# Optimization experiments

Measured on AMD Instinct MI355X. Metric: run time of the kernel, lower is better.

## Reference

```python
import math
import jax, jax.numpy as jnp
import numpy as np

HEAD_DIM = 64
N_HEAD = 8
INIT_SIZE = 1200  # -> 1201 embeddings, origin_shift = 601


def rel_sinusoidal_pos_embed(seq_len, dim=HEAD_DIM):
    """Matches RelativeSinusoidalPositionalEmbedding(dim, padding_idx=0, init_size=1200)."""
    num = INIT_SIZE + 1  # 1201
    half = dim // 2
    inv_freq = jnp.exp(jnp.arange(half, dtype=jnp.float32) * -(math.log(10000.0) / (half - 1)))
    pos = jnp.arange(-(num // 2), num // 2, dtype=jnp.float32)  # -601 .. 599 (1201 values)
    ang = pos[:, None] * inv_freq[None, :]                      # [num, half]
    w = jnp.concatenate([jnp.sin(ang), jnp.cos(ang)], axis=1)   # [num, dim]
    w = w.at[0].set(0.0)  # padding_idx row zeroed
    origin_shift = num // 2 + 1  # 601
    idx = jnp.arange(-seq_len, seq_len) + origin_shift          # [2L]
    return w[idx]                                               # [2L, dim]


def _shift(BD):
    # BD: [b, n, L, 2L] -> [b, n, L, L] (Transformer-XL skew trick)
    b, n, L, _ = BD.shape
    BD = jnp.pad(BD, ((0, 0), (0, 0), (0, 0), (0, 1)))  # [b,n,L,2L+1]
    BD = BD.reshape(b, n, 2 * L + 1, L)[:, :, :-1].reshape(b, n, L, 2 * L)
    return BD[:, :, :, L:]


def _transpose_shift(E):
    # E: [b, n, L, 2L] -> [b, n, L, L]
    b, n, L, _ = E.shape
    E = jnp.pad(E, ((0, 0), (0, 0), (0, 0), (0, 1))).reshape(b, n, 2 * L + 1, L)
    idx = jnp.arange(L) * 2 + 1
    return jnp.swapaxes(E[:, :, idx, :], -1, -2)


def setup_inputs() -> dict:
    key = jax.random.key(0)
    k1, k2, k3, k4 = jax.random.split(key, 4)
    B, L, D = 8, 512, 512
    x = jax.random.normal(k1, (B, L, D), dtype=jnp.float32)
    mask = jnp.ones((B, L), dtype=jnp.int32)
    W_qkv = jax.random.normal(k2, (D, 3 * D), dtype=jnp.float32) * (1.0 / math.sqrt(D))
    r_r_bias = jax.random.normal(k3, (N_HEAD, HEAD_DIM), dtype=jnp.float32) * 0.1
    r_w_bias = jax.random.normal(k4, (N_HEAD, HEAD_DIM), dtype=jnp.float32) * 0.1
    return {"x": x, "mask": mask, "W_qkv": W_qkv, "r_r_bias": r_r_bias, "r_w_bias": r_w_bias}


def reference(x, mask, W_qkv, r_r_bias, r_w_bias):
    B, L, D = x.shape
    scale = math.sqrt(HEAD_DIM)
    pos = rel_sinusoidal_pos_embed(L)  # [2L, head_dim], detached constant

    qkv = x @ W_qkv  # [B, L, 3D]
    q, k, v = jnp.split(qkv, 3, axis=-1)
    q = q.reshape(B, L, N_HEAD, HEAD_DIM).transpose(0, 2, 1, 3)  # [B,H,L,d]
    k = k.reshape(B, L, N_HEAD, HEAD_DIM).transpose(0, 2, 1, 3)
    v = v.reshape(B, L, N_HEAD, HEAD_DIM).transpose(0, 2, 1, 3)

    rw_head_q = q + r_r_bias[None, :, None, :]
    AC = jnp.einsum('bnqd,bnkd->bnqk', rw_head_q, k)              # [B,H,L,L]
    D_ = jnp.einsum('nd,ld->nl', r_w_bias, pos)[None, :, None, :] # [1,H,1,2L]
    B_ = jnp.einsum('bnqd,ld->bnql', q, pos)                      # [B,H,L,2L]
    E_ = jnp.einsum('bnqd,ld->bnql', k, pos)                      # [B,H,L,2L]

    BDE = _shift(B_ + D_) + _transpose_shift(E_)                  # [B,H,L,L]
    attn = (AC + BDE) / scale
    attn = jnp.where(mask[:, None, None, :] == 0, -jnp.inf, attn)
    attn = jax.nn.softmax(attn, axis=-1)

    out = jnp.matmul(attn, v)                                     # [B,H,L,d]
    return out.transpose(0, 2, 1, 3).reshape(B, L, D)
```

## Files before the change

kernel.cpp:

```cpp
#include <hip/hip_runtime.h>
#include <hip/hip_bf16.h>
#include <math.h>

#define LSEQ 512
#define DDIM 192

typedef __attribute__((ext_vector_type(8))) short s16x8;
typedef __attribute__((ext_vector_type(4))) float f32x4;
typedef unsigned short ushort_t;
typedef unsigned int uint_t;

#define MFMA16(a, b, c) __builtin_amdgcn_mfma_f32_16x16x32_bf16(a, b, c, 0, 0, 0)

__device__ __forceinline__ ushort_t f2b(float f) {
  union { float f; uint_t u; } v; v.f = f;
  uint_t r = (v.u + 0x7FFFu + ((v.u >> 16) & 1u)) >> 16;
  return (ushort_t)r;
}
__device__ __forceinline__ float b2f(ushort_t u) {
  union { uint_t u; float f; } v; v.u = ((uint_t)u) << 16;
  return v.f;
}

typedef const __attribute__((address_space(1))) void g_void_t;
typedef __attribute__((address_space(3))) void lds_void_t;
__device__ __forceinline__ void load_lds16(const void* g, void* l) {
  __builtin_amdgcn_global_load_lds((g_void_t*)g, (lds_void_t*)l, 16, 0, 0);
}

__device__ __forceinline__ size_t kswz(size_t row, int d) {
  return row * DDIM + (size_t)((d & 0x1C7) | ((((d >> 3) & 7) ^ ((int)row & 7)) << 3));
}

__global__ void cast_x(const float* __restrict__ x, ushort_t* __restrict__ xb) {
  const int i = (blockIdx.x * 256 + threadIdx.x) * 8;
  const int row = i >> 9, k = i & 511;
  float4 a = *(const float4*)(x + i);
  float4 b = *(const float4*)(x + i + 4);
  uint4 o;
  o.x = (uint_t)f2b(a.x) | ((uint_t)f2b(a.y) << 16);
  o.y = (uint_t)f2b(a.z) | ((uint_t)f2b(a.w) << 16);
  o.z = (uint_t)f2b(b.x) | ((uint_t)f2b(b.y) << 16);
  o.w = (uint_t)f2b(b.z) | ((uint_t)f2b(b.w) << 16);
  const int dst = row * 512 + (k & 448) + (((((k >> 3) & 7) ^ (row & 7))) << 3);
  *(uint4*)(xb + dst) = o;
}

__global__ void cast_transpose_w(const float* __restrict__ W, ushort_t* __restrict__ Wt) {
  __shared__ float tile[32][33];
  const int tx = threadIdx.x & 31, ty = threadIdx.x >> 5;
  const int k0 = blockIdx.x * 32, n0 = blockIdx.y * 32;
#pragma unroll
  for (int i = 0; i < 4; ++i)
    tile[ty + i * 8][tx] = W[(size_t)(k0 + ty + i * 8) * 1536 + n0 + tx];
  __syncthreads();
#pragma unroll
  for (int i = 0; i < 4; ++i) {
    const int n = n0 + ty + i * 8, k = k0 + tx;
    Wt[(size_t)n * 512 + (k & 448) + ((((k >> 3) & 7) ^ (n & 7)) << 3) + (k & 7)] =
        f2b(tile[tx][ty + i * 8]);
  }
}

__global__ __launch_bounds__(256, 3) void qkv_gemm(
    const ushort_t* __restrict__ xb, const ushort_t* __restrict__ Wt,
    const float* __restrict__ rr,
    ushort_t* __restrict__ Qt, ushort_t* __restrict__ Kt, ushort_t* __restrict__ Vt) {
  __shared__ __align__(16) ushort_t ldsA[2][64 * 64];
  __shared__ __align__(16) ushort_t ldsB[2][128 * 64];
  const int tid = threadIdx.x;
  const int w = tid >> 6, lane = tid & 63, lo = lane & 15, hi = lane >> 4;
  const int wm = w >> 1, wn = w & 1;
  const int id = blockIdx.x;
  const int mp = id & 63, np = id >> 6;
  const int m0 = mp * 64, n0 = np * 128;

  f32x4 acc[2][4];
  const f32x4 zero4 = {0.f, 0.f, 0.f, 0.f};
#pragma unroll
  for (int i = 0; i < 2; ++i)
#pragma unroll
    for (int j = 0; j < 4; ++j) acc[i][j] = zero4;

  const char* asrc = (const char*)xb + (size_t)m0 * 1024;
  const char* bsrc = (const char*)Wt + (size_t)n0 * 1024;

#define STAGE_QKV(buf, ks)                                                     \
  {                                                                            \
    char* la = (char*)&ldsA[buf][0] + w * 1024;                                \
    char* lb = (char*)&ldsB[buf][0] + w * 1024;                                \
    _Pragma("unroll") for (int it = 0; it < 2; ++it) {                         \
      const int X = it * 4096 + tid * 16;                                      \
      load_lds16(asrc + (size_t)(X >> 7) * 1024 + (ks) * 128 + (X & 127),      \
                 la + it * 4096);                                              \
    }                                                                          \
    _Pragma("unroll") for (int it = 0; it < 4; ++it) {                         \
      const int X = it * 4096 + tid * 16;                                      \
      load_lds16(bsrc + (size_t)(X >> 7) * 1024 + (ks) * 128 + (X & 127),      \
                 lb + it * 4096);                                              \
    }                                                                          \
  }

  STAGE_QKV(0, 0);
  for (int ks = 0; ks < 8; ++ks) {
    const int cur = ks & 1;
    __syncthreads();
    if (ks < 7) STAGE_QKV(cur ^ 1, ks + 1);
    const char* Ab = (const char*)&ldsA[cur][0];
    const char* Bb = (const char*)&ldsB[cur][0];
#pragma unroll
    for (int kh = 0; kh < 2; ++kh) {
      const int sw = ((kh * 4 + hi) ^ (lo & 7)) << 4;
      s16x8 a[2], bf[4];
#pragma unroll
      for (int i = 0; i < 2; ++i)
        a[i] = *(const s16x8*)(Ab + (wm * 32 + i * 16 + lo) * 128 + sw);
#pragma unroll
      for (int j = 0; j < 4; ++j)
        bf[j] = *(const s16x8*)(Bb + (wn * 64 + j * 16 + lo) * 128 + sw);
#pragma unroll
      for (int i = 0; i < 2; ++i)
#pragma unroll
        for (int j = 0; j < 4; ++j)
          acc[i][j] = MFMA16(a[i], bf[j], acc[i][j]);
    }
  }

  const int sect = n0 >> 9;
  const int h = ((n0 + wn * 64) >> 6) & 7;
  const int mrow0 = m0 + wm * 32;

  if (sect == 0) {
    float bias[4];
#pragma unroll
    for (int j = 0; j < 4; ++j) bias[j] = rr[h * 64 + j * 16 + lo];
#pragma unroll
    for (int i = 0; i < 2; ++i)
#pragma unroll
      for (int r = 0; r < 4; ++r) {
        const int m = mrow0 + i * 16 + hi * 4 + r;
        const size_t row = ((size_t)(m >> 9) * 8 + h) * 512 + (m & 511);
#pragma unroll
        for (int j = 0; j < 4; ++j)
          Qt[row * DDIM + j * 16 + lo] = f2b((acc[i][j][r] + bias[j]) * 0.125f);
      }
  } else if (sect == 1) {
#pragma unroll
    for (int i = 0; i < 2; ++i)
#pragma unroll
      for (int r = 0; r < 4; ++r) {
        const int m = mrow0 + i * 16 + hi * 4 + r;
        const size_t row = ((size_t)(m >> 9) * 8 + h) * 512 + (m & 511);
#pragma unroll
        for (int j = 0; j < 4; ++j)
          Kt[row * DDIM + ((((j * 2 + (lo >> 3)) ^ (m & 7)) << 3) | (lo & 7))] =
              f2b(acc[i][j][r]);
      }
  } else {
#pragma unroll
    for (int i = 0; i < 2; ++i) {
      const int b = (mrow0 + i * 16) >> 9;
      const int l0 = (mrow0 + i * 16 + hi * 4) & 511;
#pragma unroll
      for (int j = 0; j < 4; ++j) {
        ushort4 pk;
        pk.x = f2b(acc[i][j][0]); pk.y = f2b(acc[i][j][1]);
        pk.z = f2b(acc[i][j][2]); pk.w = f2b(acc[i][j][3]);
        *(ushort4*)&Vt[(((size_t)b * 8 + h) * 64 + j * 16 + lo) * 512 + l0] = pk;
      }
    }
  }
}

__global__ void build_feats(ushort_t* __restrict__ Qt, ushort_t* __restrict__ Kt,
                            const float* __restrict__ rr, const float* __restrict__ rw) {
  const int idx = blockIdx.x * blockDim.x + threadIdx.x;
  const int hf = idx & 31;
  const size_t row = (size_t)(idx >> 5);
  const int l = (int)(row & 511);
  const int hh = (int)((row >> 9) & 7);

  const float f = __expf(-(float)hf * 0.29710775393472f);
  float s0, c0, s1, c1;
  __sincosf((float)l * f, &s0, &c0);
  __sincosf((float)(l + 1) * f, &s1, &c1);

  const size_t qb = row * DDIM;
  const float qr_s = b2f(Qt[qb + hf]);
  const float qr_c = b2f(Qt[qb + 32 + hf]);
  const float qw_s = qr_s + 0.125f * (rw[hh * 64 + hf] - rr[hh * 64 + hf]);
  const float qw_c = qr_c + 0.125f * (rw[hh * 64 + 32 + hf] - rr[hh * 64 + 32 + hf]);
  Qt[qb + 64 + hf]  = f2b(qw_s * c0 + qw_c * s0);
  Qt[qb + 96 + hf]  = f2b(qw_c * c0 - qw_s * s0);
  Qt[qb + 128 + hf] = f2b(0.125f * s1);
  Qt[qb + 160 + hf] = f2b(0.125f * c1);

  const float k_s = b2f(Kt[kswz(row, hf)]);
  const float k_c = b2f(Kt[kswz(row, 32 + hf)]);
  Kt[kswz(row, 64 + hf)]  = f2b(s1);
  Kt[kswz(row, 96 + hf)]  = f2b(c1);
  Kt[kswz(row, 128 + hf)] = f2b(k_s * c0 + k_c * s0);
  Kt[kswz(row, 160 + hf)] = f2b(k_c * c0 - k_s * s0);
}

__global__ __launch_bounds__(256, 2) void attn_kernel(
    const ushort_t* __restrict__ Qt, const ushort_t* __restrict__ Kt,
    const ushort_t* __restrict__ Vt, const int* __restrict__ mask,
    float* __restrict__ out) {
  __shared__ __align__(16) ushort_t ldsK[2][64 * DDIM];
  __shared__ __align__(16) ushort_t P[4][16][72];

  const int tid = threadIdx.x;
  const int w = tid >> 6;
  const int lane = tid & 63, lo = lane & 15, hi = lane >> 4;
  const int id = blockIdx.x;
  const int bh = id & 63, qg = id >> 6;
  const int b = bh >> 3, h = bh & 7;
  const int q0 = qg * 64 + w * 16;
  const size_t qrow0 = (size_t)bh * LSEQ + q0;

  s16x8 qf[6];
#pragma unroll
  for (int ks = 0; ks < 6; ++ks)
    qf[ks] = *(const s16x8*)(Qt + (qrow0 + lo) * DDIM + ks * 32 + hi * 8);

  const f32x4 zero4 = {0.f, 0.f, 0.f, 0.f};
  f32x4 o[4];
#pragma unroll
  for (int j = 0; j < 4; ++j) o[j] = zero4;
  float mrun = -3.0e38f, lrun = 0.f;

  const char* ksrc = (const char*)(Kt + (size_t)bh * LSEQ * DDIM);
  const ushort_t* vbase = Vt + ((size_t)bh * 64 + lo) * 512 + hi * 8;

  {
    char* d = (char*)&ldsK[0][0] + w * 1024;
#pragma unroll
    for (int it = 0; it < 6; ++it)
      load_lds16(ksrc + it * 4096 + tid * 16, d + it * 4096);
  }

  for (int kt = 0; kt < 8; ++kt) {
    const int cur = kt & 1;
    __syncthreads();
    if (kt < 7) {
      const char* s = ksrc + (kt + 1) * 24576;
      char* d = (char*)&ldsK[cur ^ 1][0] + w * 1024;
#pragma unroll
      for (int it = 0; it < 6; ++it)
        load_lds16(s + it * 4096 + tid * 16, d + it * 4096);
    }

    f32x4 sf[4];
#pragma unroll
    for (int f = 0; f < 4; ++f) sf[f] = zero4;
    const char* kl = (const char*)&ldsK[cur][0];
    __builtin_amdgcn_s_setprio(1);
#pragma unroll
    for (int ks = 0; ks < 6; ++ks) {
      const int swb = ((ks * 4 + hi) ^ (lo & 7)) << 4;
#pragma unroll
      for (int f = 0; f < 4; ++f) {
        s16x8 ka = *(const s16x8*)(kl + (f * 16 + lo) * 384 + swb);
        sf[f] = MFMA16(ka, qf[ks], sf[f]);
      }
    }
    __builtin_amdgcn_s_setprio(0);

    const int mk = mask[b * LSEQ + kt * 64 + lane];
    if (__ballot(mk == 0) != 0ull) {
#pragma unroll
      for (int f = 0; f < 4; ++f)
#pragma unroll
        for (int r = 0; r < 4; ++r)
          if (__shfl(mk, f * 16 + hi * 4 + r) == 0) sf[f][r] = -3.0e38f;
    }

    float tm = fmaxf(fmaxf(sf[0][0], sf[0][1]), fmaxf(sf[0][2], sf[0][3]));
#pragma unroll
    for (int f = 1; f < 4; ++f)
      tm = fmaxf(tm, fmaxf(fmaxf(sf[f][0], sf[f][1]), fmaxf(sf[f][2], sf[f][3])));
    tm = fmaxf(tm, __shfl_xor(tm, 16));
    tm = fmaxf(tm, __shfl_xor(tm, 32));

    if (!__all(tm - mrun <= 8.0f)) {
      const float mnew = fmaxf(mrun, tm);
      const float corr = __expf(mrun - mnew);
      lrun *= corr;
      mrun = mnew;
      float cq[4];
#pragma unroll
      for (int r = 0; r < 4; ++r) cq[r] = __shfl(corr, hi * 4 + r);
#pragma unroll
      for (int j = 0; j < 4; ++j)
#pragma unroll
        for (int r = 0; r < 4; ++r) o[j][r] *= cq[r];
    }

    float ts = 0.f;
#pragma unroll
    for (int f = 0; f < 4; ++f)
#pragma unroll
      for (int r = 0; r < 4; ++r) {
        sf[f][r] = __expf(sf[f][r] - mrun);
        ts += sf[f][r];
      }
    ts += __shfl_xor(ts, 16);
    ts += __shfl_xor(ts, 32);
    lrun += ts;

#pragma unroll
    for (int f = 0; f < 4; ++f) {
      __hip_bfloat162 p0 = __float22bfloat162_rn(make_float2(sf[f][0], sf[f][1]));
      __hip_bfloat162 p1 = __float22bfloat162_rn(make_float2(sf[f][2], sf[f][3]));
      uint2 u;
      __builtin_memcpy(&u.x, &p0, 4);
      __builtin_memcpy(&u.y, &p1, 4);
      *(uint2*)&P[w][lo][f * 16 + hi * 4] = u;
    }

    __builtin_amdgcn_s_setprio(1);
#pragma unroll
    for (int kh = 0; kh < 2; ++kh) {
      s16x8 pa = *(const s16x8*)&P[w][lo][kh * 32 + hi * 8];
#pragma unroll
      for (int j = 0; j < 4; ++j) {
        s16x8 vb = *(const s16x8*)(vbase + (size_t)j * 16 * 512 + kt * 64 + kh * 32);
        o[j] = MFMA16(pa, vb, o[j]);
      }
    }
    __builtin_amdgcn_s_setprio(0);
  }

  float lq[4];
#pragma unroll
  for (int r = 0; r < 4; ++r) lq[r] = 1.0f / __shfl(lrun, hi * 4 + r);
#pragma unroll
  for (int j = 0; j < 4; ++j)
#pragma unroll
    for (int r = 0; r < 4; ++r)
      out[((size_t)b * LSEQ + q0 + hi * 4 + r) * 512 + h * 64 + j * 16 + lo] =
          o[j][r] * lq[r];
}

extern "C" void kernel_launch(void* const* d_in, const int* in_sizes, int n_in,
                              void* d_out, int out_size, void* d_ws, size_t ws_size,
                              hipStream_t stream) {
  const float* x    = (const float*)d_in[0];
  const int*   mask = (const int*)d_in[1];
  const float* W    = (const float*)d_in[2];
  const float* rr   = (const float*)d_in[3];
  const float* rw   = (const float*)d_in[4];
  float* out = (float*)d_out;

  char* ws = (char*)d_ws;
  ushort_t* xb = (ushort_t*)(ws);
  ushort_t* Wt = (ushort_t*)(ws + 4194304);
  ushort_t* Qt = (ushort_t*)(ws + 5767168);
  ushort_t* Kt = (ushort_t*)(ws + 18350080);
  ushort_t* Vt = (ushort_t*)(ws + 30932992);

  cast_x<<<1024, 256, 0, stream>>>(x, xb);
  cast_transpose_w<<<dim3(16, 48), 256, 0, stream>>>(W, Wt);
  qkv_gemm<<<768, 256, 0, stream>>>(xb, Wt, rr, Qt, Kt, Vt);
  build_feats<<<4096, 256, 0, stream>>>(Qt, Kt, rr, rw);
  attn_kernel<<<512, 256, 0, stream>>>(Qt, Kt, Vt, mask, out);
}
```

Measured before the change: 60.75 us.

## Fuse cast kernels, fold feature build into QKV GEMM epilogue, prefetch V

The two cast kernels become a single launch, and the positional-feature construction (the separate build_feats pass) moves into the QKV GEMM epilogue, which now writes the sin/cos-rotated Q and K columns directly. The GEMM tile grows from 64x128 to 128x128 with fewer blocks and launch bounds lowered to 2 waves per SIMD. The attention kernel now loads the V fragments and mask before the barrier so the global loads overlap the QK compute. This removes two launches and a read-modify-write pass over Q and K, at the cost of higher register pressure and a smaller GEMM grid (384 blocks).

```diff
diff --git a/kernel.cpp b/kernel.cpp
--- a/kernel.cpp
+++ b/kernel.cpp
@@ -17,10 +17,6 @@
   uint_t r = (v.u + 0x7FFFu + ((v.u >> 16) & 1u)) >> 16;
   return (ushort_t)r;
 }
-__device__ __forceinline__ float b2f(ushort_t u) {
-  union { uint_t u; float f; } v; v.u = ((uint_t)u) << 16;
-  return v.f;
-}
 
 typedef const __attribute__((address_space(1))) void g_void_t;
 typedef __attribute__((address_space(3))) void lds_void_t;
@@ -32,53 +28,56 @@
   return row * DDIM + (size_t)((d & 0x1C7) | ((((d >> 3) & 7) ^ ((int)row & 7)) << 3));
 }
 
-__global__ void cast_x(const float* __restrict__ x, ushort_t* __restrict__ xb) {
-  const int i = (blockIdx.x * 256 + threadIdx.x) * 8;
-  const int row = i >> 9, k = i & 511;
-  float4 a = *(const float4*)(x + i);
-  float4 b = *(const float4*)(x + i + 4);
-  uint4 o;
-  o.x = (uint_t)f2b(a.x) | ((uint_t)f2b(a.y) << 16);
-  o.y = (uint_t)f2b(a.z) | ((uint_t)f2b(a.w) << 16);
-  o.z = (uint_t)f2b(b.x) | ((uint_t)f2b(b.y) << 16);
-  o.w = (uint_t)f2b(b.z) | ((uint_t)f2b(b.w) << 16);
-  const int dst = row * 512 + (k & 448) + (((((k >> 3) & 7) ^ (row & 7))) << 3);
-  *(uint4*)(xb + dst) = o;
-}
-
-__global__ void cast_transpose_w(const float* __restrict__ W, ushort_t* __restrict__ Wt) {
+__global__ void cast_all(const float* __restrict__ x, const float* __restrict__ W,
+                         ushort_t* __restrict__ xb, ushort_t* __restrict__ Wt) {
   __shared__ float tile[32][33];
-  const int tx = threadIdx.x & 31, ty = threadIdx.x >> 5;
-  const int k0 = blockIdx.x * 32, n0 = blockIdx.y * 32;
-#pragma unroll
-  for (int i = 0; i < 4; ++i)
-    tile[ty + i * 8][tx] = W[(size_t)(k0 + ty + i * 8) * 1536 + n0 + tx];
-  __syncthreads();
-#pragma unroll
-  for (int i = 0; i < 4; ++i) {
-    const int n = n0 + ty + i * 8, k = k0 + tx;
-    Wt[(size_t)n * 512 + (k & 448) + ((((k >> 3) & 7) ^ (n & 7)) << 3) + (k & 7)] =
-        f2b(tile[tx][ty + i * 8]);
-  }
-}
-
-__global__ __launch_bounds__(256, 3) void qkv_gemm(
+  const int id = blockIdx.x;
+  if (id < 1024) {
+    const int i = (id * 256 + threadIdx.x) * 8;
+    const int row = i >> 9, k = i & 511;
+    float4 a = *(const float4*)(x + i);
+    float4 b = *(const float4*)(x + i + 4);
+    uint4 o;
+    o.x = (uint_t)f2b(a.x) | ((uint_t)f2b(a.y) << 16);
+    o.y = (uint_t)f2b(a.z) | ((uint_t)f2b(a.w) << 16);
+    o.z = (uint_t)f2b(b.x) | ((uint_t)f2b(b.y) << 16);
+    o.w = (uint_t)f2b(b.z) | ((uint_t)f2b(b.w) << 16);
+    const int dst = row * 512 + (k & 448) + (((((k >> 3) & 7) ^ (row & 7))) << 3);
+    *(uint4*)(xb + dst) = o;
+  } else {
+    const int wid = id - 1024;
+    const int tx = threadIdx.x & 31, ty = threadIdx.x >> 5;
+    const int k0 = (wid & 15) * 32, n0 = (wid >> 4) * 32;
+#pragma unroll
+    for (int i = 0; i < 4; ++i)
+      tile[ty + i * 8][tx] = W[(size_t)(k0 + ty + i * 8) * 1536 + n0 + tx];
+    __syncthreads();
+#pragma unroll
+    for (int i = 0; i < 4; ++i) {
+      const int n = n0 + ty + i * 8, k = k0 + tx;
+      Wt[(size_t)n * 512 + (k & 448) + ((((k >> 3) & 7) ^ (n & 7)) << 3) + (k & 7)] =
+          f2b(tile[tx][ty + i * 8]);
+    }
+  }
+}
+
+__global__ __launch_bounds__(256, 2) void qkv_gemm(
     const ushort_t* __restrict__ xb, const ushort_t* __restrict__ Wt,
-    const float* __restrict__ rr,
+    const float* __restrict__ rr, const float* __restrict__ rw,
     ushort_t* __restrict__ Qt, ushort_t* __restrict__ Kt, ushort_t* __restrict__ Vt) {
-  __shared__ __align__(16) ushort_t ldsA[2][64 * 64];
+  __shared__ __align__(16) ushort_t ldsA[2][128 * 64];
   __shared__ __align__(16) ushort_t ldsB[2][128 * 64];
   const int tid = threadIdx.x;
   const int w = tid >> 6, lane = tid & 63, lo = lane & 15, hi = lane >> 4;
   const int wm = w >> 1, wn = w & 1;
   const int id = blockIdx.x;
-  const int mp = id & 63, np = id >> 6;
-  const int m0 = mp * 64, n0 = np * 128;
-
-  f32x4 acc[2][4];
+  const int mp = id & 31, np = id >> 5;
+  const int m0 = mp * 128, n0 = np * 128;
+
+  f32x4 acc[4][4];
   const f32x4 zero4 = {0.f, 0.f, 0.f, 0.f};
 #pragma unroll
-  for (int i = 0; i < 2; ++i)
+  for (int i = 0; i < 4; ++i)
 #pragma unroll
     for (int j = 0; j < 4; ++j) acc[i][j] = zero4;
 
@@ -87,17 +86,14 @@
 
 #define STAGE_QKV(buf, ks)                                                     \
   {                                                                            \
-    char* la = (char*)&ldsA[buf][0] + w * 1024;                                \
-    char* lb = (char*)&ldsB[buf][0] + w * 1024;                                \
-    _Pragma("unroll") for (int it = 0; it < 2; ++it) {                         \
+    char* la = (char*)&ldsA[buf][0];                                           \
+    char* lb = (char*)&ldsB[buf][0];                                           \
+    _Pragma("unroll") for (int it = 0; it < 4; ++it) {                         \
       const int X = it * 4096 + tid * 16;                                      \
       load_lds16(asrc + (size_t)(X >> 7) * 1024 + (ks) * 128 + (X & 127),      \
-                 la + it * 4096);                                              \
-    }                                                                          \
-    _Pragma("unroll") for (int it = 0; it < 4; ++it) {                         \
-      const int X = it * 4096 + tid * 16;                                      \
+                 la + X);                                                      \
       load_lds16(bsrc + (size_t)(X >> 7) * 1024 + (ks) * 128 + (X & 127),      \
-                 lb + it * 4096);                                              \
+                 lb + X);                                                      \
     }                                                                          \
   }
 
@@ -111,56 +107,32 @@
 #pragma unroll
     for (int kh = 0; kh < 2; ++kh) {
       const int sw = ((kh * 4 + hi) ^ (lo & 7)) << 4;
-      s16x8 a[2], bf[4];
-#pragma unroll
-      for (int i = 0; i < 2; ++i)
-        a[i] = *(const s16x8*)(Ab + (wm * 32 + i * 16 + lo) * 128 + sw);
+      s16x8 a[4], bf[4];
+#pragma unroll
+      for (int i = 0; i < 4; ++i)
+        a[i] = *(const s16x8*)(Ab + (wm * 64 + i * 16 + lo) * 128 + sw);
 #pragma unroll
       for (int j = 0; j < 4; ++j)
         bf[j] = *(const s16x8*)(Bb + (wn * 64 + j * 16 + lo) * 128 + sw);
 #pragma unroll
-      for (int i = 0; i < 2; ++i)
+      for (int i = 0; i < 4; ++i)
 #pragma unroll
         for (int j = 0; j < 4; ++j)
           acc[i][j] = MFMA16(a[i], bf[j], acc[i][j]);
     }
   }
 
-  const int sect = n0 >> 9;
-  const int h = ((n0 + wn * 64) >> 6) & 7;
-  const int mrow0 = m0 + wm * 32;
-
-  if (sect == 0) {
-    float bias[4];
-#pragma unroll
-    for (int j = 0; j < 4; ++j) bias[j] = rr[h * 64 + j * 16 + lo];
-#pragma unroll
-    for (int i = 0; i < 2; ++i)
-#pragma unroll
-      for (int r = 0; r < 4; ++r) {
-        const int m = mrow0 + i * 16 + hi * 4 + r;
-        const size_t row = ((size_t)(m >> 9) * 8 + h) * 512 + (m & 511);
-#pragma unroll
-        for (int j = 0; j < 4; ++j)
-          Qt[row * DDIM + j * 16 + lo] = f2b((acc[i][j][r] + bias[j]) * 0.125f);
-      }
-  } else if (sect == 1) {
-#pragma unroll
-    for (int i = 0; i < 2; ++i)
-#pragma unroll
-      for (int r = 0; r < 4; ++r) {
-        const int m = mrow0 + i * 16 + hi * 4 + r;
-        const size_t row = ((size_t)(m >> 9) * 8 + h) * 512 + (m & 511);
-#pragma unroll
-        for (int j = 0; j < 4; ++j)
-          Kt[row * DDIM + ((((j * 2 + (lo >> 3)) ^ (m & 7)) << 3) | (lo & 7))] =
-              f2b(acc[i][j][r]);
-      }
-  } else {
-#pragma unroll
-    for (int i = 0; i < 2; ++i) {
-      const int b = (mrow0 + i * 16) >> 9;
-      const int l0 = (mrow0 + i * 16 + hi * 4) & 511;
+  const int gn0 = n0 + wn * 64;
+  const int sect = gn0 >> 9;
+  const int h = (gn0 >> 6) & 7;
+  const int mrow0 = m0 + wm * 64;
+
+  if (sect == 2) {
+#pragma unroll
+    for (int i = 0; i < 4; ++i) {
+      const int m16 = mrow0 + i * 16;
+      const int b = m16 >> 9;
+      const int l0 = (m16 + hi * 4) & 511;
 #pragma unroll
       for (int j = 0; j < 4; ++j) {
         ushort4 pk;
@@ -169,38 +141,64 @@
         *(ushort4*)&Vt[(((size_t)b * 8 + h) * 64 + j * 16 + lo) * 512 + l0] = pk;
       }
     }
-  }
-}
-
-__global__ void build_feats(ushort_t* __restrict__ Qt, ushort_t* __restrict__ Kt,
-                            const float* __restrict__ rr, const float* __restrict__ rw) {
-  const int idx = blockIdx.x * blockDim.x + threadIdx.x;
-  const int hf = idx & 31;
-  const size_t row = (size_t)(idx >> 5);
-  const int l = (int)(row & 511);
-  const int hh = (int)((row >> 9) & 7);
-
-  const float f = __expf(-(float)hf * 0.29710775393472f);
-  float s0, c0, s1, c1;
-  __sincosf((float)l * f, &s0, &c0);
-  __sincosf((float)(l + 1) * f, &s1, &c1);
-
-  const size_t qb = row * DDIM;
-  const float qr_s = b2f(Qt[qb + hf]);
-  const float qr_c = b2f(Qt[qb + 32 + hf]);
-  const float qw_s = qr_s + 0.125f * (rw[hh * 64 + hf] - rr[hh * 64 + hf]);
-  const float qw_c = qr_c + 0.125f * (rw[hh * 64 + 32 + hf] - rr[hh * 64 + 32 + hf]);
-  Qt[qb + 64 + hf]  = f2b(qw_s * c0 + qw_c * s0);
-  Qt[qb + 96 + hf]  = f2b(qw_c * c0 - qw_s * s0);
-  Qt[qb + 128 + hf] = f2b(0.125f * s1);
-  Qt[qb + 160 + hf] = f2b(0.125f * c1);
-
-  const float k_s = b2f(Kt[kswz(row, hf)]);
-  const float k_c = b2f(Kt[kswz(row, 32 + hf)]);
-  Kt[kswz(row, 64 + hf)]  = f2b(s1);
-  Kt[kswz(row, 96 + hf)]  = f2b(c1);
-  Kt[kswz(row, 128 + hf)] = f2b(k_s * c0 + k_c * s0);
-  Kt[kswz(row, 160 + hf)] = f2b(k_c * c0 - k_s * s0);
+  } else if (sect == 0) {
+#pragma unroll
+    for (int p = 0; p < 2; ++p) {
+      const int hf = p * 16 + lo;
+      const float rrs = rr[h * 64 + hf], rrc = rr[h * 64 + 32 + hf];
+      const float rws = rw[h * 64 + hf], rwc = rw[h * 64 + 32 + hf];
+      const float fq = __expf(-(float)hf * 0.29710775393472f);
+      float sfr, cfr;
+      __sincosf(fq, &sfr, &cfr);
+#pragma unroll
+      for (int i = 0; i < 4; ++i)
+#pragma unroll
+        for (int r = 0; r < 4; ++r) {
+          const int m = mrow0 + i * 16 + hi * 4 + r;
+          const int l = m & 511;
+          const size_t base = (((size_t)(m >> 9) * 8 + h) * 512 + l) * DDIM;
+          float s0, c0;
+          __sincosf((float)l * fq, &s0, &c0);
+          const float s1 = s0 * cfr + c0 * sfr;
+          const float c1 = c0 * cfr - s0 * sfr;
+          const float vs = acc[i][p][r], vc = acc[i][p + 2][r];
+          const float qs = (vs + rws) * 0.125f, qc = (vc + rwc) * 0.125f;
+          Qt[base + hf]       = f2b((vs + rrs) * 0.125f);
+          Qt[base + 32 + hf]  = f2b((vc + rrc) * 0.125f);
+          Qt[base + 64 + hf]  = f2b(qs * c0 + qc * s0);
+          Qt[base + 96 + hf]  = f2b(qc * c0 - qs * s0);
+          Qt[base + 128 + hf] = f2b(0.125f * s1);
+          Qt[base + 160 + hf] = f2b(0.125f * c1);
+        }
+    }
+  } else {
+#pragma unroll
+    for (int p = 0; p < 2; ++p) {
+      const int hf = p * 16 + lo;
+      const float fq = __expf(-(float)hf * 0.29710775393472f);
+      float sfr, cfr;
+      __sincosf(fq, &sfr, &cfr);
+#pragma unroll
+      for (int i = 0; i < 4; ++i)
+#pragma unroll
+        for (int r = 0; r < 4; ++r) {
+          const int m = mrow0 + i * 16 + hi * 4 + r;
+          const int l = m & 511;
+          const size_t row = ((size_t)(m >> 9) * 8 + h) * 512 + l;
+          float s0, c0;
+          __sincosf((float)l * fq, &s0, &c0);
+          const float s1 = s0 * cfr + c0 * sfr;
+          const float c1 = c0 * cfr - s0 * sfr;
+          const float ks_ = acc[i][p][r], kc_ = acc[i][p + 2][r];
+          Kt[kswz(row, hf)]       = f2b(ks_);
+          Kt[kswz(row, 32 + hf)]  = f2b(kc_);
+          Kt[kswz(row, 64 + hf)]  = f2b(s1);
+          Kt[kswz(row, 96 + hf)]  = f2b(c1);
+          Kt[kswz(row, 128 + hf)] = f2b(ks_ * c0 + kc_ * s0);
+          Kt[kswz(row, 160 + hf)] = f2b(kc_ * c0 - ks_ * s0);
+        }
+    }
+  }
 }
 
 __global__ __launch_bounds__(256, 2) void attn_kernel(
@@ -233,22 +231,32 @@
   const char* ksrc = (const char*)(Kt + (size_t)bh * LSEQ * DDIM);
   const ushort_t* vbase = Vt + ((size_t)bh * 64 + lo) * 512 + hi * 8;
 
-  {
-    char* d = (char*)&ldsK[0][0] + w * 1024;
-#pragma unroll
-    for (int it = 0; it < 6; ++it)
-      load_lds16(ksrc + it * 4096 + tid * 16, d + it * 4096);
+#pragma unroll
+  for (int it = 0; it < 6; ++it) {
+    const int X = it * 4096 + tid * 16;
+    load_lds16(ksrc + X, (char*)&ldsK[0][0] + X);
   }
 
   for (int kt = 0; kt < 8; ++kt) {
     const int cur = kt & 1;
+
+    const int mk = mask[b * LSEQ + kt * 64 + lane];
+    s16x8 vbf[2][4];
+#pragma unroll
+    for (int kh = 0; kh < 2; ++kh)
+#pragma unroll
+      for (int j = 0; j < 4; ++j)
+        vbf[kh][j] = *(const s16x8*)(vbase + (size_t)j * 16 * 512 + kt * 64 + kh * 32);
+
     __syncthreads();
     if (kt < 7) {
       const char* s = ksrc + (kt + 1) * 24576;
-      char* d = (char*)&ldsK[cur ^ 1][0] + w * 1024;
-#pragma unroll
-      for (int it = 0; it < 6; ++it)
-        load_lds16(s + it * 4096 + tid * 16, d + it * 4096);
+      char* d = (char*)&ldsK[cur ^ 1][0];
+#pragma unroll
+      for (int it = 0; it < 6; ++it) {
+        const int X = it * 4096 + tid * 16;
+        load_lds16(s + X, d + X);
+      }
     }
 
     f32x4 sf[4];
@@ -267,7 +275,6 @@
     }
     __builtin_amdgcn_s_setprio(0);
 
-    const int mk = mask[b * LSEQ + kt * 64 + lane];
     if (__ballot(mk == 0) != 0ull) {
 #pragma unroll
       for (int f = 0; f < 4; ++f)
@@ -324,10 +331,8 @@
     for (int kh = 0; kh < 2; ++kh) {
       s16x8 pa = *(const s16x8*)&P[w][lo][kh * 32 + hi * 8];
 #pragma unroll
-      for (int j = 0; j < 4; ++j) {
-        s16x8 vb = *(const s16x8*)(vbase + (size_t)j * 16 * 512 + kt * 64 + kh * 32);
-        o[j] = MFMA16(pa, vb, o[j]);
-      }
+      for (int j = 0; j < 4; ++j)
+        o[j] = MFMA16(pa, vbf[kh][j], o[j]);
     }
     __builtin_amdgcn_s_setprio(0);
   }
@@ -360,9 +365,7 @@
   ushort_t* Kt = (ushort_t*)(ws + 18350080);
   ushort_t* Vt = (ushort_t*)(ws + 30932992);
 
-  cast_x<<<1024, 256, 0, stream>>>(x, xb);
-  cast_transpose_w<<<dim3(16, 48), 256, 0, stream>>>(W, Wt);
-  qkv_gemm<<<768, 256, 0, stream>>>(xb, Wt, rr, Qt, Kt, Vt);
-  build_feats<<<4096, 256, 0, stream>>>(Qt, Kt, rr, rw);
+  cast_all<<<1792, 256, 0, stream>>>(x, W, xb, Wt);
+  qkv_gemm<<<384, 256, 0, stream>>>(xb, Wt, rr, rw, Qt, Kt, Vt);
   attn_kernel<<<512, 256, 0, stream>>>(Qt, Kt, Vt, mask, out);
 }
```

Result: faster. 53.35 us (-12.2%).
